# Optimization experiments

Measured on AMD Instinct MI355X. Metric: run time of the kernel, lower is better.

Reference implementation:

```python
import jax, jax.numpy as jnp
import numpy as np

BS, N_LINKS, MAX_LEN = 8192, 512, 32
D_LINK, D_PATH, D_READ, N_OUT = 32, 128, 256, 3
BN_EPS = 1e-5


def setup_inputs() -> dict:
    key = jax.random.key(0)
    ks = jax.random.split(key, 16)
    capa = jax.random.uniform(ks[0], (BS, N_LINKS), jnp.float32, 0.5, 1.0) * 100.0
    avail = jax.random.uniform(ks[1], (BS, N_LINKS), jnp.float32) * capa
    loss = jax.random.uniform(ks[2], (BS, N_LINKS), jnp.float32) * 0.05
    demand = jax.random.uniform(ks[3], (BS,), jnp.float32) * 10.0
    path = jax.random.randint(ks[4], (BS, MAX_LEN), 0, N_LINKS)
    hop_num = jax.random.randint(ks[5], (BS,), 1, MAX_LEN + 1)
    s = 0.1
    inp = {
        "demand": demand,
        "link_avail_capacity": avail,
        "link_capacity": capa,
        "link_loss": loss,
        "path": path,
        "hop_num": hop_num,
        # GRU params (PyTorch layout: [3H, D] gates ordered r,z,n)
        "gru_w_ih": jax.random.normal(ks[6], (3 * D_PATH, D_LINK), jnp.float32) * s,
        "gru_w_hh": jax.random.normal(ks[7], (3 * D_PATH, D_PATH), jnp.float32) * s,
        "gru_b_ih": jax.random.normal(ks[8], (3 * D_PATH,), jnp.float32) * s,
        "gru_b_hh": jax.random.normal(ks[9], (3 * D_PATH,), jnp.float32) * s,
        "bn_gamma": jnp.ones((D_PATH,), jnp.float32),
        "bn_beta": jnp.zeros((D_PATH,), jnp.float32),
        # stacked readout heads [N_OUT, ...]
        "rW1": jax.random.normal(ks[10], (N_OUT, D_PATH, D_READ), jnp.float32) * s,
        "rb1": jnp.zeros((N_OUT, D_READ), jnp.float32),
        "rW2": jax.random.normal(ks[11], (N_OUT, D_READ, D_READ), jnp.float32) * s,
        "rb2": jnp.zeros((N_OUT, D_READ), jnp.float32),
        "rW3": jax.random.normal(ks[12], (N_OUT, D_READ, 1), jnp.float32) * s,
        "rb3": jnp.zeros((N_OUT, 1), jnp.float32),
    }
    return inp


def _gru_scan(x_bt, h0, w_ih, w_hh, b_ih, b_hh):
    # x_bt: [B, T, D]; h0: [B, H] -> outputs [B, T, H]
    H = h0.shape[-1]
    def step(h, x_t):
        gi = x_t @ w_ih.T + b_ih          # [B, 3H]
        gh = h @ w_hh.T + b_hh            # [B, 3H]
        i_r, i_z, i_n = gi[:, :H], gi[:, H:2*H], gi[:, 2*H:]
        h_r, h_z, h_n = gh[:, :H], gh[:, H:2*H], gh[:, 2*H:]
        r = jax.nn.sigmoid(i_r + h_r)
        z = jax.nn.sigmoid(i_z + h_z)
        n = jnp.tanh(i_n + r * h_n)
        h_new = (1.0 - z) * n + z * h
        return h_new, h_new
    _, outs = jax.lax.scan(step, h0, jnp.swapaxes(x_bt, 0, 1))
    return jnp.swapaxes(outs, 0, 1)


def reference(demand, link_avail_capacity, link_capacity, link_loss, path, hop_num,
              gru_w_ih, gru_w_hh, gru_b_ih, gru_b_hh, bn_gamma, bn_beta,
              rW1, rb1, rW2, rb2, rW3, rb3):
    bs, n_links = link_capacity.shape
    max_len = path.shape[1]
    max_capa = jax.lax.stop_gradient(jnp.max(link_capacity))
    # link_state: [B, n_links, D_LINK]; first D_LINK-4 channels are zeros
    feats = jnp.stack([
        link_avail_capacity / max_capa,
        link_capacity / max_capa,
        link_avail_capacity / link_capacity,
        link_loss,
    ], axis=-1)
    link_state = jnp.concatenate(
        [jnp.zeros((bs, n_links, D_LINK - 4), feats.dtype), feats], axis=-1)
    link_state = jax.lax.stop_gradient(link_state)  # original detaches
    # initial hidden: zeros except last channel = demand/max_capa
    h0 = jnp.concatenate(
        [jnp.zeros((bs, D_PATH - 1), feats.dtype), (demand / max_capa)[:, None]], axis=-1)
    # fused gather of link states along each path, masked past hop_num
    gathered = jnp.take_along_axis(link_state, path[:, :, None], axis=1)  # [B, T, D]
    mask = (jnp.arange(max_len)[None, :] < hop_num[:, None])[:, :, None]
    link_inputs = gathered * mask.astype(gathered.dtype)
    outputs = _gru_scan(link_inputs, h0, gru_w_ih, gru_w_hh, gru_b_ih, gru_b_hh)
    # extract hidden state at last hop of each path
    idx = (hop_num - 1)[:, None, None]
    flow = jnp.take_along_axis(outputs, idx, axis=1)[:, 0, :]  # [B, H]
    # BatchNorm1d (training mode: batch statistics, biased variance)
    mean = jnp.mean(flow, axis=0)
    var = jnp.mean((flow - mean) ** 2, axis=0)
    flow = (flow - mean) * jax.lax.rsqrt(var + BN_EPS) * bn_gamma + bn_beta
    # readout heads: Linear -> SELU -> Linear -> SELU -> Linear
    h1 = jax.nn.selu(jnp.einsum('bh,uhr->ubr', flow, rW1) + rb1[:, None, :])
    h2 = jax.nn.selu(jnp.einsum('ubr,urs->ubs', h1, rW2) + rb2[:, None, :])
    y = jnp.einsum('ubs,uso->ubo', h2, rW3) + rb3[:, None, :]  # [U, B, 1]
    return jnp.transpose(y[:, :, 0], (1, 0))  # [B, U]
```

## Files before the change

### kernel.cpp

```cpp
#include <hip/hip_runtime.h>


#define BS 8192
#define NL 512
#define ML 32
#define DP 128
#define DR 256
#define NJOB 512
#define ST 172

#define OFF_SUM    64
#define OFF_SSQ    192
#define OFF_CUR    576
#define OFF_PERM   640
#define OFF_WHH16  (OFF_PERM + BS)
#define OFF_W1     (OFF_WHH16 + 24576)
#define OFF_W2     (OFF_W1 + 49152)
#define OFF_FEATS  (OFF_W2 + 98304)
#define OFF_FLOW   (OFF_FEATS + BS*ML*4)

#define FEATS_BLOCKS 1024
#define MAX_BLOCKS   256
#define WPREP_BLOCKS 336
#define SORT_BID     (FEATS_BLOCKS + MAX_BLOCKS + WPREP_BLOCKS)
#define PREP_GRID    (SORT_BID + 1)

#define KS (-1.44269504088896340736f)
#define KT ( 2.88539008177792681472f)

typedef _Float16 f16x8 __attribute__((ext_vector_type(8)));
typedef _Float16 f16x4 __attribute__((ext_vector_type(4)));
typedef float    f32x4 __attribute__((ext_vector_type(4)));

__device__ __forceinline__ float sig2_(float x){
  return __builtin_amdgcn_rcpf(1.0f + exp2f(x));
}
__device__ __forceinline__ float tanh2_(float v){
  return fmaf(-2.0f, __builtin_amdgcn_rcpf(1.0f + exp2f(v)), 1.0f);
}
__device__ __forceinline__ float seluf_(float x){
  const float sc = 1.0507009873554805f, al = 1.6732632423543772f;
  return x > 0.0f ? sc*x : sc*al*(__expf(x)-1.0f);
}

__global__ void prep_all(const int* __restrict__ path, const int* __restrict__ hop,
                         const float* __restrict__ avail, const float* __restrict__ capa,
                         const float* __restrict__ loss, const float* __restrict__ whh,
                         const float* __restrict__ rW1, const float* __restrict__ rW2,
                         float* ws){
  const int bid = blockIdx.x;
  const int tid = threadIdx.x;

  if (bid < FEATS_BLOCKS){
    int idx = bid*256 + tid;
    int b = idx >> 5, t = idx & 31;
    f16x4 o = (f16x4)0;
    if (t < hop[b]){
      int l = path[idx];
      float a = avail[b*NL + l];
      float c = capa [b*NL + l];
      o[0] = (_Float16)a;
      o[1] = (_Float16)c;
      o[2] = (_Float16)(a / c);
      o[3] = (_Float16)loss[b*NL + l];
    }
    ((f16x4*)((_Float16*)(ws + OFF_FEATS)))[idx] = o;
  } else if (bid < FEATS_BLOCKS + MAX_BLOCKS){
    const float4* c4 = (const float4*)capa;
    const int n4 = BS*NL/4;
    float m = 0.0f;
    for (int i = (bid - FEATS_BLOCKS)*256 + tid; i < n4; i += MAX_BLOCKS*256){
      float4 v = c4[i];
      m = fmaxf(m, fmaxf(fmaxf(v.x, v.y), fmaxf(v.z, v.w)));
    }
    #pragma unroll
    for (int o = 32; o > 0; o >>= 1) m = fmaxf(m, __shfl_down(m, o, 64));
    if ((tid & 63) == 0) atomicMax((int*)ws, __float_as_int(m));
  } else if (bid < SORT_BID){
    _Float16* whh16 = (_Float16*)(ws + OFF_WHH16);
    _Float16* w1    = (_Float16*)(ws + OFF_W1);
    _Float16* w2    = (_Float16*)(ws + OFF_W2);
    int base = (bid - FEATS_BLOCKS - MAX_BLOCKS)*1024 + tid*4;
    if (base < 49152){
      const float s = (base < 32768) ? KS : KT;
      const float4 v = *(const float4*)(whh + base);
      f16x4 o = { (_Float16)(v.x*s), (_Float16)(v.y*s),
                  (_Float16)(v.z*s), (_Float16)(v.w*s) };
      *(f16x4*)(whh16 + base) = o;
    } else if (base < 147456){
      int j = base - 49152; int u = j >> 15; int rem = j & 32767; int n = rem >> 7; int k = rem & 127;
      const float* src = rW1 + u*32768 + k*256 + n;
      f16x4 o = { (_Float16)src[0], (_Float16)src[256], (_Float16)src[512], (_Float16)src[768] };
      *(f16x4*)(w1 + j) = o;
    } else {
      int j = base - 147456; int u = j >> 16; int rem = j & 65535; int n = rem >> 8; int k = rem & 255;
      const float* src = rW2 + u*65536 + k*256 + n;
      f16x4 o = { (_Float16)src[0], (_Float16)src[256], (_Float16)src[512], (_Float16)src[768] };
      *(f16x4*)(w2 + j) = o;
    }
  } else {
    __shared__ int hist[32], start[32];
    for (int i = 64 + tid; i < 640; i += 256) ws[i] = 0.0f;
    if (tid < 32) hist[tid] = 0;
    __syncthreads();
    for (int b = tid; b < BS; b += 256) atomicAdd(&hist[32 - hop[b]], 1);
    __syncthreads();
    if (tid == 0){ int acc = 0; for (int i = 0; i < 32; ++i){ start[i] = acc; acc += hist[i]; } }
    __syncthreads();
    int* perm = (int*)ws + OFF_PERM;
    for (int b = tid; b < BS; b += 256){
      int pos = atomicAdd(&start[32 - hop[b]], 1);
      perm[pos] = b;
    }
  }
}

__launch_bounds__(512, 4)
__global__ void kgru(const float* __restrict__ demand, const int* __restrict__ hop,
                     const float* __restrict__ wih, const float* __restrict__ bih,
                     const float* __restrict__ bhh, float* __restrict__ ws,
                     float* __restrict__ flow){
  __shared__ _Float16 hA[2][16*ST];
  const int tid  = threadIdx.x;
  const int w    = tid >> 6;
  const int lane = tid & 63;
  const int lm   = lane & 15;
  const int qd   = lane >> 4;
  const int ch   = w*16 + lm;
  const float inv_maxc = 1.0f / ws[0];
  const int* perm = (const int*)ws + OFF_PERM;
  const f16x4* feats16 = (const f16x4*)((const _Float16*)(ws + OFF_FEATS));
  const _Float16* whh16 = (const _Float16*)(ws + OFF_WHH16);

  const int bid = blockIdx.x;
  const int q = (bid < 256) ? bid : 767 - bid;

  for (int idx = tid; idx < 1024; idx += 512){
    const int buf = idx >> 9;
    const int rem = idx & 511;
    const int m   = rem >> 5;
    const int c   = 128 + (rem & 31);
    hA[buf][m*ST + c] = (_Float16)0.f;
  }

  f16x8 bfr[5], bfz[5], bfnh[4], bfni;
  #pragma unroll
  for (int kc = 0; kc < 4; ++kc){
    bfr[kc]  = *(const f16x8*)(whh16 + (      ch)*128 + kc*32 + qd*8);
    bfz[kc]  = *(const f16x8*)(whh16 + (128 + ch)*128 + kc*32 + qd*8);
    bfnh[kc] = *(const f16x8*)(whh16 + (256 + ch)*128 + kc*32 + qd*8);
  }
  bfr[4] = (f16x8)0; bfz[4] = (f16x8)0; bfni = (f16x8)0;
  if (qd == 0){
    #pragma unroll
    for (int j = 0; j < 4; ++j){
      float s = (j < 2) ? inv_maxc : 1.0f;
      bfr[4][j] = (_Float16)(wih[(      ch)*32 + 28 + j] * s * KS);
      bfz[4][j] = (_Float16)(wih[(128 + ch)*32 + 28 + j] * s * KS);
      bfni[j]   = (_Float16)(wih[(256 + ch)*32 + 28 + j] * s * KT);
    }
  }
  const float bR  = (bih[ch]     + bhh[ch]    ) * KS;
  const float bZ  = (bih[128+ch] + bhh[128+ch]) * KS;
  const float bNI = bih[256+ch] * KT;
  const float bNH = bhh[256+ch] * KT;

  int it[4], hp[4];
  #pragma unroll
  for (int r = 0; r < 4; ++r){
    it[r] = perm[q*16 + qd*4 + r];
    hp[r] = hop[it[r]];
  }
  int tmax = max(max(hp[0],hp[1]), max(hp[2],hp[3]));
  tmax = max(tmax, __shfl_xor(tmax, 16, 64));
  tmax = max(tmax, __shfl_xor(tmax, 32, 64));

  const int  fw_i = w*2 + lane;
  const bool fw   = (lane < 2);
  const int  fw_b = fw ? perm[q*16 + fw_i] : 0;

  __syncthreads();

  float hprev[4];
  #pragma unroll
  for (int r = 0; r < 4; ++r){
    float h0 = (ch == 127) ? demand[it[r]] * inv_maxc : 0.0f;
    hprev[r] = h0;
    hA[0][(qd*4 + r)*ST + ch] = (_Float16)h0;
  }
  if (fw)
    *(f16x4*)(&hA[0][fw_i*ST + 128]) = feats16[fw_b*ML + 0];
  __syncthreads();

  for (int t = 0; t < tmax; ++t){
    const int cur = t & 1, nxt = cur ^ 1;
    if (fw && (t+1) < ML)
      *(f16x4*)(&hA[nxt][fw_i*ST + 128]) = feats16[fw_b*ML + t + 1];

    f32x4 accr  = {bR, bR, bR, bR};
    f32x4 accz  = {bZ, bZ, bZ, bZ};
    f32x4 accnh = {bNH, bNH, bNH, bNH};
    f32x4 accni = {bNI, bNI, bNI, bNI};
    #pragma unroll
    for (int kc = 0; kc < 5; ++kc){
      f16x8 a = *(const f16x8*)(&hA[cur][lm*ST + kc*32 + qd*8]);
      accr = __builtin_amdgcn_mfma_f32_16x16x32_f16(a, bfr[kc], accr, 0, 0, 0);
      accz = __builtin_amdgcn_mfma_f32_16x16x32_f16(a, bfz[kc], accz, 0, 0, 0);
      if (kc < 4)
        accnh = __builtin_amdgcn_mfma_f32_16x16x32_f16(a, bfnh[kc], accnh, 0, 0, 0);
      else
        accni = __builtin_amdgcn_mfma_f32_16x16x32_f16(a, bfni, accni, 0, 0, 0);
    }

    #pragma unroll
    for (int r = 0; r < 4; ++r){
      float rr = sig2_(accr[r]);
      float zz = sig2_(accz[r]);
      float nn = tanh2_(fmaf(rr, accnh[r], accni[r]));
      float hn = fmaf(zz, hprev[r] - nn, nn);
      if (t < hp[r]) hprev[r] = hn;
      hA[nxt][(qd*4 + r)*ST + ch] = (_Float16)hprev[r];
    }
    __syncthreads();
  }

  float ssum = 0.f, ssq = 0.f;
  #pragma unroll
  for (int r = 0; r < 4; ++r){
    float v = hprev[r];
    flow[it[r]*DP + ch] = v;
    ssum += v;
    ssq  = fmaf(v, v, ssq);
  }
  ssum += __shfl_xor(ssum, 16, 64);  ssum += __shfl_xor(ssum, 32, 64);
  ssq  += __shfl_xor(ssq,  16, 64);  ssq  += __shfl_xor(ssq,  32, 64);
  if (qd == 0){
    atomicAdd(&ws[OFF_SUM + ch], ssum);
    atomicAdd(&ws[OFF_SSQ + ch], ssq);
  }
}

__launch_bounds__(256, 4)
__global__ void kmlp(const float* __restrict__ flow, const float* __restrict__ ws,
                     const float* __restrict__ gamma, const float* __restrict__ beta,
                     const float* __restrict__ rb1, const float* __restrict__ rb2,
                     const float* __restrict__ rW3, const float* __restrict__ rb3,
                     float* __restrict__ out){
  __shared__ _Float16 x_lds[32*136];
  __shared__ _Float16 h1_lds[32*264];
  __shared__ float aa[DP], bb[DP];
  __shared__ float y_part[4][32];
  const int tid  = threadIdx.x;
  const int w    = tid >> 6;
  const int lane = tid & 63;
  const int lm   = lane & 15;
  const int qd   = lane >> 4;
  const int b0   = blockIdx.x * 32;
  const int u    = blockIdx.y;
  const _Float16* w1 = (const _Float16*)(ws + OFF_W1) + u*(DR*DP);
  const _Float16* w2 = (const _Float16*)(ws + OFF_W2) + u*(DR*DR);

  if (tid < DP){
    float m = ws[OFF_SUM + tid] * (1.0f/BS);
    float q = ws[OFF_SSQ + tid] * (1.0f/BS);
    float rstd = rsqrtf(q - m*m + 1e-5f);
    float a = rstd * gamma[tid];
    aa[tid] = a;
    bb[tid] = fmaf(-m, a, beta[tid]);
  }
  __syncthreads();

  for (int idx = tid; idx < 32*DP; idx += 256){
    int i = idx >> 7, h = idx & 127;
    x_lds[i*136 + h] = (_Float16)fmaf(flow[(b0 + i)*DP + h], aa[h], bb[h]);
  }
  __syncthreads();

  for (int nt = 0; nt < 4; ++nt){
    const int n = (4*w + nt)*16 + lm;
    const float bias1 = rb1[u*DR + n];
    f16x8 b1[4];
    #pragma unroll
    for (int kc = 0; kc < 4; ++kc)
      b1[kc] = *(const f16x8*)(w1 + n*DP + kc*32 + qd*8);
    #pragma unroll
    for (int mt = 0; mt < 2; ++mt){
      f32x4 acc = {bias1, bias1, bias1, bias1};
      #pragma unroll
      for (int kc = 0; kc < 4; ++kc){
        f16x8 a1 = *(const f16x8*)(&x_lds[(mt*16 + lm)*136 + kc*32 + qd*8]);
        acc = __builtin_amdgcn_mfma_f32_16x16x32_f16(a1, b1[kc], acc, 0, 0, 0);
      }
      #pragma unroll
      for (int r = 0; r < 4; ++r)
        h1_lds[(mt*16 + qd*4 + r)*264 + n] = (_Float16)seluf_(acc[r]);
    }
  }
  __syncthreads();

  {
    float p[2][4] = {{0.f,0.f,0.f,0.f},{0.f,0.f,0.f,0.f}};
    for (int nt = 0; nt < 4; ++nt){
      const int n = (4*w + nt)*16 + lm;
      const float bias2 = rb2[u*DR + n];
      const float w3l   = rW3[u*DR + n];
      f16x8 b2[8];
      #pragma unroll
      for (int kc = 0; kc < 8; ++kc)
        b2[kc] = *(const f16x8*)(w2 + n*DR + kc*32 + qd*8);
      #pragma unroll
      for (int mt = 0; mt < 2; ++mt){
        f32x4 acc = {bias2, bias2, bias2, bias2};
        #pragma unroll
        for (int kc = 0; kc < 8; ++kc){
          f16x8 a2 = *(const f16x8*)(&h1_lds[(mt*16 + lm)*264 + kc*32 + qd*8]);
          acc = __builtin_amdgcn_mfma_f32_16x16x32_f16(a2, b2[kc], acc, 0, 0, 0);
        }
        #pragma unroll
        for (int r = 0; r < 4; ++r)
          p[mt][r] += seluf_(acc[r]) * w3l;
      }
    }
    #pragma unroll
    for (int mt = 0; mt < 2; ++mt){
      #pragma unroll
      for (int r = 0; r < 4; ++r){
        float v = p[mt][r];
        v += __shfl_xor(v, 1, 64);
        v += __shfl_xor(v, 2, 64);
        v += __shfl_xor(v, 4, 64);
        v += __shfl_xor(v, 8, 64);
        if (lm == 0) y_part[w][mt*16 + qd*4 + r] = v;
      }
    }
  }
  __syncthreads();
  if (tid < 32){
    float y = y_part[0][tid] + y_part[1][tid] + y_part[2][tid] + y_part[3][tid] + rb3[u];
    out[(b0 + tid)*3 + u] = y;
  }
}

extern "C" void kernel_launch(void* const* d_in, const int* in_sizes, int n_in,
                              void* d_out, int out_size, void* d_ws, size_t ws_size,
                              hipStream_t stream){
  const float* demand = (const float*)d_in[0];
  const float* avail  = (const float*)d_in[1];
  const float* capa   = (const float*)d_in[2];
  const float* loss   = (const float*)d_in[3];
  const int*   path   = (const int*)d_in[4];
  const int*   hop    = (const int*)d_in[5];
  const float* wih    = (const float*)d_in[6];
  const float* whh    = (const float*)d_in[7];
  const float* bih    = (const float*)d_in[8];
  const float* bhh    = (const float*)d_in[9];
  const float* gamma  = (const float*)d_in[10];
  const float* beta   = (const float*)d_in[11];
  const float* rW1    = (const float*)d_in[12];
  const float* rb1    = (const float*)d_in[13];
  const float* rW2    = (const float*)d_in[14];
  const float* rb2    = (const float*)d_in[15];
  const float* rW3    = (const float*)d_in[16];
  const float* rb3    = (const float*)d_in[17];
  float* ws  = (float*)d_ws;
  float* out = (float*)d_out;

  prep_all <<<PREP_GRID, 256, 0, stream>>>(path, hop, avail, capa, loss,
                                           whh, rW1, rW2, ws);
  kgru     <<<NJOB, 512, 0, stream>>>(demand, hop, wih, bih, bhh, ws, ws + OFF_FLOW);
  kmlp     <<<dim3(BS/32, 3), 256, 0, stream>>>(ws + OFF_FLOW, ws, gamma, beta,
                                                rb1, rb2, rW3, rb3, out);
}
```

Before: 200.4 us.

## Transpose GRU MFMA operands so each lane owns one path and four channels

The MFMA operand order is swapped so the accumulator holds four consecutive hidden channels for a single path per lane, rather than one channel across four paths. This allows packed f16x4 writes of the hidden state to LDS, float4 stores of flow, a single per-lane hop mask, and float4 bias loads. Feature loads are now software-prefetched one step ahead into registers. The BN statistics reduction becomes a 16-lane butterfly over eight values followed by more atomics per wave. Together these aim to cut LDS store instructions and global load latency inside the serial recurrence.

```diff
diff --git a/kernel.cpp b/kernel.cpp
--- a/kernel.cpp
+++ b/kernel.cpp
@@ -126,7 +126,8 @@
   const int lane = tid & 63;
   const int lm   = lane & 15;
   const int qd   = lane >> 4;
-  const int ch   = w*16 + lm;
+  const int chw  = w*16 + lm;
+  const int cho  = w*16 + qd*4;
   const float inv_maxc = 1.0f / ws[0];
   const int* perm = (const int*)ws + OFF_PERM;
   const f16x4* feats16 = (const f16x4*)((const _Float16*)(ws + OFF_FEATS));
@@ -146,34 +147,40 @@
   f16x8 bfr[5], bfz[5], bfnh[4], bfni;
   #pragma unroll
   for (int kc = 0; kc < 4; ++kc){
-    bfr[kc]  = *(const f16x8*)(whh16 + (      ch)*128 + kc*32 + qd*8);
-    bfz[kc]  = *(const f16x8*)(whh16 + (128 + ch)*128 + kc*32 + qd*8);
-    bfnh[kc] = *(const f16x8*)(whh16 + (256 + ch)*128 + kc*32 + qd*8);
+    bfr[kc]  = *(const f16x8*)(whh16 + (      chw)*128 + kc*32 + qd*8);
+    bfz[kc]  = *(const f16x8*)(whh16 + (128 + chw)*128 + kc*32 + qd*8);
+    bfnh[kc] = *(const f16x8*)(whh16 + (256 + chw)*128 + kc*32 + qd*8);
   }
   bfr[4] = (f16x8)0; bfz[4] = (f16x8)0; bfni = (f16x8)0;
   if (qd == 0){
     #pragma unroll
     for (int j = 0; j < 4; ++j){
       float s = (j < 2) ? inv_maxc : 1.0f;
-      bfr[4][j] = (_Float16)(wih[(      ch)*32 + 28 + j] * s * KS);
-      bfz[4][j] = (_Float16)(wih[(128 + ch)*32 + 28 + j] * s * KS);
-      bfni[j]   = (_Float16)(wih[(256 + ch)*32 + 28 + j] * s * KT);
-    }
-  }
-  const float bR  = (bih[ch]     + bhh[ch]    ) * KS;
-  const float bZ  = (bih[128+ch] + bhh[128+ch]) * KS;
-  const float bNI = bih[256+ch] * KT;
-  const float bNH = bhh[256+ch] * KT;
-
-  int it[4], hp[4];
-  #pragma unroll
-  for (int r = 0; r < 4; ++r){
-    it[r] = perm[q*16 + qd*4 + r];
-    hp[r] = hop[it[r]];
-  }
-  int tmax = max(max(hp[0],hp[1]), max(hp[2],hp[3]));
-  tmax = max(tmax, __shfl_xor(tmax, 16, 64));
-  tmax = max(tmax, __shfl_xor(tmax, 32, 64));
+      bfr[4][j] = (_Float16)(wih[(      chw)*32 + 28 + j] * s * KS);
+      bfz[4][j] = (_Float16)(wih[(128 + chw)*32 + 28 + j] * s * KS);
+      bfni[j]   = (_Float16)(wih[(256 + chw)*32 + 28 + j] * s * KT);
+    }
+  }
+  const float4 biR = *(const float4*)(bih + cho);
+  const float4 bhR = *(const float4*)(bhh + cho);
+  const float4 biZ = *(const float4*)(bih + 128 + cho);
+  const float4 bhZ = *(const float4*)(bhh + 128 + cho);
+  const float4 biN = *(const float4*)(bih + 256 + cho);
+  const float4 bhN = *(const float4*)(bhh + 256 + cho);
+  const f32x4 cR  = { (biR.x+bhR.x)*KS, (biR.y+bhR.y)*KS,
+                      (biR.z+bhR.z)*KS, (biR.w+bhR.w)*KS };
+  const f32x4 cZ  = { (biZ.x+bhZ.x)*KS, (biZ.y+bhZ.y)*KS,
+                      (biZ.z+bhZ.z)*KS, (biZ.w+bhZ.w)*KS };
+  const f32x4 cNI = { biN.x*KT, biN.y*KT, biN.z*KT, biN.w*KT };
+  const f32x4 cNH = { bhN.x*KT, bhN.y*KT, bhN.z*KT, bhN.w*KT };
+
+  const int it = perm[q*16 + lm];
+  const int hp = hop[it];
+  int tmax = hp;
+  tmax = max(tmax, __shfl_xor(tmax, 1, 64));
+  tmax = max(tmax, __shfl_xor(tmax, 2, 64));
+  tmax = max(tmax, __shfl_xor(tmax, 4, 64));
+  tmax = max(tmax, __shfl_xor(tmax, 8, 64));
 
   const int  fw_i = w*2 + lane;
   const bool fw   = (lane < 2);
@@ -181,62 +188,81 @@
 
   __syncthreads();
 
-  float hprev[4];
-  #pragma unroll
-  for (int r = 0; r < 4; ++r){
-    float h0 = (ch == 127) ? demand[it[r]] * inv_maxc : 0.0f;
-    hprev[r] = h0;
-    hA[0][(qd*4 + r)*ST + ch] = (_Float16)h0;
-  }
-  if (fw)
+  float hprev[4] = {0.f, 0.f, 0.f, 0.f};
+  if (w == 7 && qd == 3) hprev[3] = demand[it] * inv_maxc;
+  {
+    f16x4 pk = { (_Float16)hprev[0], (_Float16)hprev[1],
+                 (_Float16)hprev[2], (_Float16)hprev[3] };
+    *(f16x4*)(&hA[0][lm*ST + cho]) = pk;
+  }
+  f16x4 fvreg = (f16x4)0;
+  if (fw){
     *(f16x4*)(&hA[0][fw_i*ST + 128]) = feats16[fw_b*ML + 0];
+    fvreg = feats16[fw_b*ML + 1];
+  }
   __syncthreads();
 
   for (int t = 0; t < tmax; ++t){
     const int cur = t & 1, nxt = cur ^ 1;
-    if (fw && (t+1) < ML)
-      *(f16x4*)(&hA[nxt][fw_i*ST + 128]) = feats16[fw_b*ML + t + 1];
-
-    f32x4 accr  = {bR, bR, bR, bR};
-    f32x4 accz  = {bZ, bZ, bZ, bZ};
-    f32x4 accnh = {bNH, bNH, bNH, bNH};
-    f32x4 accni = {bNI, bNI, bNI, bNI};
+
+    f16x4 fvnext = fvreg;
+    if (fw){
+      *(f16x4*)(&hA[nxt][fw_i*ST + 128]) = fvreg;
+      int tn = t + 2; tn = (tn < ML) ? tn : (ML - 1);
+      fvnext = feats16[fw_b*ML + tn];
+    }
+
+    f32x4 accr = cR, accz = cZ, accnh = cNH, accni = cNI;
     #pragma unroll
     for (int kc = 0; kc < 5; ++kc){
       f16x8 a = *(const f16x8*)(&hA[cur][lm*ST + kc*32 + qd*8]);
-      accr = __builtin_amdgcn_mfma_f32_16x16x32_f16(a, bfr[kc], accr, 0, 0, 0);
-      accz = __builtin_amdgcn_mfma_f32_16x16x32_f16(a, bfz[kc], accz, 0, 0, 0);
+      accr = __builtin_amdgcn_mfma_f32_16x16x32_f16(bfr[kc], a, accr, 0, 0, 0);
+      accz = __builtin_amdgcn_mfma_f32_16x16x32_f16(bfz[kc], a, accz, 0, 0, 0);
       if (kc < 4)
-        accnh = __builtin_amdgcn_mfma_f32_16x16x32_f16(a, bfnh[kc], accnh, 0, 0, 0);
+        accnh = __builtin_amdgcn_mfma_f32_16x16x32_f16(bfnh[kc], a, accnh, 0, 0, 0);
       else
-        accni = __builtin_amdgcn_mfma_f32_16x16x32_f16(a, bfni, accni, 0, 0, 0);
-    }
-
+        accni = __builtin_amdgcn_mfma_f32_16x16x32_f16(bfni, a, accni, 0, 0, 0);
+    }
+
+    const bool upd = (t < hp);
+    f16x4 pk;
     #pragma unroll
     for (int r = 0; r < 4; ++r){
       float rr = sig2_(accr[r]);
       float zz = sig2_(accz[r]);
       float nn = tanh2_(fmaf(rr, accnh[r], accni[r]));
       float hn = fmaf(zz, hprev[r] - nn, nn);
-      if (t < hp[r]) hprev[r] = hn;
-      hA[nxt][(qd*4 + r)*ST + ch] = (_Float16)hprev[r];
-    }
+      if (upd) hprev[r] = hn;
+      pk[r] = (_Float16)hprev[r];
+    }
+    *(f16x4*)(&hA[nxt][lm*ST + cho]) = pk;
+    fvreg = fvnext;
     __syncthreads();
   }
 
-  float ssum = 0.f, ssq = 0.f;
+  {
+    float4 fo = { hprev[0], hprev[1], hprev[2], hprev[3] };
+    *(float4*)(&flow[it*DP + cho]) = fo;
+  }
+  float sv0 = hprev[0], sv1 = hprev[1], sv2 = hprev[2], sv3 = hprev[3];
+  float qv0 = hprev[0]*hprev[0], qv1 = hprev[1]*hprev[1];
+  float qv2 = hprev[2]*hprev[2], qv3 = hprev[3]*hprev[3];
   #pragma unroll
-  for (int r = 0; r < 4; ++r){
-    float v = hprev[r];
-    flow[it[r]*DP + ch] = v;
-    ssum += v;
-    ssq  = fmaf(v, v, ssq);
-  }
-  ssum += __shfl_xor(ssum, 16, 64);  ssum += __shfl_xor(ssum, 32, 64);
-  ssq  += __shfl_xor(ssq,  16, 64);  ssq  += __shfl_xor(ssq,  32, 64);
-  if (qd == 0){
-    atomicAdd(&ws[OFF_SUM + ch], ssum);
-    atomicAdd(&ws[OFF_SSQ + ch], ssq);
+  for (int o = 1; o < 16; o <<= 1){
+    sv0 += __shfl_xor(sv0, o, 64);  qv0 += __shfl_xor(qv0, o, 64);
+    sv1 += __shfl_xor(sv1, o, 64);  qv1 += __shfl_xor(qv1, o, 64);
+    sv2 += __shfl_xor(sv2, o, 64);  qv2 += __shfl_xor(qv2, o, 64);
+    sv3 += __shfl_xor(sv3, o, 64);  qv3 += __shfl_xor(qv3, o, 64);
+  }
+  if (lm == 0){
+    atomicAdd(&ws[OFF_SUM + cho + 0], sv0);
+    atomicAdd(&ws[OFF_SUM + cho + 1], sv1);
+    atomicAdd(&ws[OFF_SUM + cho + 2], sv2);
+    atomicAdd(&ws[OFF_SUM + cho + 3], sv3);
+    atomicAdd(&ws[OFF_SSQ + cho + 0], qv0);
+    atomicAdd(&ws[OFF_SSQ + cho + 1], qv1);
+    atomicAdd(&ws[OFF_SSQ + cho + 2], qv2);
+    atomicAdd(&ws[OFF_SSQ + cho + 3], qv3);
   }
 }
 
```

New measurement: 229.6 us. 1.15x slower.
